# Performance work log

Measured on AMD Instinct MI355X. Metric: run time of the kernel, lower is better.

The kernel has to match this reference:

```python
import jax, jax.numpy as jnp
import numpy as np

BSZ, D = 256, 512
LOGIT_SCALE = 1.0


def setup_inputs() -> dict:
    key = jax.random.key(0)
    k1, k2, k3 = jax.random.split(key, 3)
    x = jax.random.normal(k1, (BSZ, D), dtype=jnp.float32)
    y = jax.random.normal(k2, (BSZ, D), dtype=jnp.float32)
    z = jax.random.normal(k3, (BSZ, D), dtype=jnp.float32)
    return {"x": x, "y": y, "z": z}


def _logits_n_squared(anchor, a, b, shift):
    # torch recursion: products[i*bsz + r] = a[r] * roll(b, i)[r] = a[r] * b[(r - i) % bsz]
    bsz = anchor.shape[0]
    P = a[None, :, :] * b[shift]              # (i, r, d) = (bsz, bsz, d)
    logits = jnp.einsum('ad,ird->air', anchor, P)  # (a, i, r)
    return LOGIT_SCALE * logits.reshape(bsz, bsz * bsz)


def _cross_entropy_diag(logits):
    bsz = logits.shape[0]
    lp = jax.nn.log_softmax(logits, axis=-1)
    idx = jnp.arange(bsz)
    return -jnp.mean(lp[idx, idx])


def reference(x, y, z):
    bsz = x.shape[0]
    r = jnp.arange(bsz)
    shift = (r[None, :] - r[:, None]) % bsz   # (i, r): index into b after roll by i
    reps = [x, y, z]
    losses = []
    for i in range(3):
        anchor = reps[i]
        non_anchor = [reps[j] for j in range(3) if j != i]
        logits = _logits_n_squared(anchor, non_anchor[0], non_anchor[1], shift)
        losses.append(_cross_entropy_diag(logits))
    return sum(losses) / 3.0
```

## Files before the change

### kernel.cpp

```cpp
#include <hip/hip_runtime.h>

#define DIM 512
#define BK 32
#define ASTRIDE 40

typedef unsigned int uint;
typedef unsigned short ushort;
typedef __attribute__((ext_vector_type(8))) short short8;
typedef __attribute__((ext_vector_type(4))) float f32x4;

__device__ __forceinline__ uint pack_bf16(float a, float b) {
    union { float f; uint u; } ua, ub;
    ua.f = a; ub.f = b;
    uint x0 = ua.u + 0x8000u;
    uint x1 = ub.u + 0x8000u;
    return __builtin_amdgcn_perm(x1, x0, 0x07060302);
}

__global__ void zconv_kernel(const float* __restrict__ z, ushort* __restrict__ zb) {
    int t = blockIdx.x * 256 + threadIdx.x;
    int f = t * 8;
    float4 a = *(const float4*)(z + f);
    float4 b = *(const float4*)(z + f + 4);
    uint4 o;
    o.x = pack_bf16(a.x, a.y);
    o.y = pack_bf16(a.z, a.w);
    o.z = pack_bf16(b.x, b.y);
    o.w = pack_bf16(b.z, b.w);
    *(uint4*)(zb + f) = o;
}

__global__ void __launch_bounds__(512, 4)
gemm_fused(const float* __restrict__ x, const float* __restrict__ y,
           const ushort* __restrict__ zb, const float* __restrict__ z,
           float* __restrict__ rowM, float* __restrict__ rowS,
           float* __restrict__ colM, float* __restrict__ colS,
           float* __restrict__ diag, uint* __restrict__ counter) {
    __shared__ __align__(16) float xs[DIM];
    __shared__ __align__(16) ushort As[128 * ASTRIDE];
    __shared__ __align__(16) ushort Bs[256 * BK];
    __shared__ float redA[128 * 4];
    __shared__ float rowMaxS[128];
    __shared__ float redB[256 * 2];
    __shared__ float colMaxS[256];
    __shared__ float dred[8];

    const int tid = threadIdx.x;
    const int a   = blockIdx.x >> 1;
    const int rt  = blockIdx.x & 1;

    if (blockIdx.x == 0 && tid == 0) *counter = 0u;

    xs[tid] = x[a * DIM + tid];

    const int lane = tid & 63;
    const int wave = tid >> 6;
    const int quad = lane >> 4;
    const int ln15 = lane & 15;
    const int wr = wave >> 2;
    const int wc = wave & 3;

    if (rt == 0) {
        float p = xs[tid] * y[a * DIM + tid] * z[a * DIM + tid];
        #pragma unroll
        for (int m = 1; m < 64; m <<= 1) p += __shfl_xor(p, m, 64);
        if (lane == 0) dred[wave] = p;
        __syncthreads();
        if (tid == 0) {
            float s = 0.f;
            #pragma unroll
            for (int w2 = 0; w2 < 8; ++w2) s += dred[w2];
            diag[a] = s;
        }
    }

    f32x4 acc[4][4];
    #pragma unroll
    for (int i = 0; i < 4; ++i)
        #pragma unroll
        for (int j = 0; j < 4; ++j)
            acc[i][j] = (f32x4){0.f, 0.f, 0.f, 0.f};

    const int rA = tid >> 2;
    const int kA = (tid & 3) * 8;
    const float* yrow = y + (rt * 128 + rA) * DIM + kA;

    const int s0 = wave * 128 + lane;
    const int row0 = s0 >> 2, kc0 = ((s0 & 3) - (row0 >> 1)) & 3;
    const ushort* gB0 = zb + row0 * DIM + kc0 * 8;
    const int s1 = s0 + 64;
    const int row1 = s1 >> 2, kc1 = ((s1 & 3) - (row1 >> 1)) & 3;
    const ushort* gB1 = zb + row1 * DIM + kc1 * 8;

    for (int kt = 0; kt < DIM / BK; ++kt) {
        const int k0 = kt * BK;
        __syncthreads();
        __builtin_amdgcn_global_load_lds(
            (const __attribute__((address_space(1))) void*)(gB0 + k0),
            (__attribute__((address_space(3))) void*)(Bs + wave * 1024), 16, 0, 0);
        __builtin_amdgcn_global_load_lds(
            (const __attribute__((address_space(1))) void*)(gB1 + k0),
            (__attribute__((address_space(3))) void*)(Bs + wave * 1024 + 512), 16, 0, 0);
        {
            float4 y0 = *(const float4*)(yrow + k0);
            float4 y1 = *(const float4*)(yrow + k0 + 4);
            float4 x0 = *(const float4*)(xs + k0 + kA);
            float4 x1 = *(const float4*)(xs + k0 + kA + 4);
            uint4 o;
            o.x = pack_bf16(y0.x * x0.x, y0.y * x0.y);
            o.y = pack_bf16(y0.z * x0.z, y0.w * x0.w);
            o.z = pack_bf16(y1.x * x1.x, y1.y * x1.y);
            o.w = pack_bf16(y1.z * x1.z, y1.w * x1.w);
            *(uint4*)(As + rA * ASTRIDE + kA) = o;
        }
        __syncthreads();
        short8 af[4], bfr[4];
        #pragma unroll
        for (int i = 0; i < 4; ++i)
            af[i] = *(const short8*)(As + (wr * 64 + i * 16 + ln15) * ASTRIDE + quad * 8);
        #pragma unroll
        for (int j = 0; j < 4; ++j) {
            int row = wc * 64 + j * 16 + ln15;
            int pos = row * 4 + ((quad + (row >> 1)) & 3);
            bfr[j] = *(const short8*)(Bs + pos * 8);
        }
        #pragma unroll
        for (int i = 0; i < 4; ++i)
            #pragma unroll
            for (int j = 0; j < 4; ++j)
                acc[i][j] = __builtin_amdgcn_mfma_f32_16x16x32_bf16(af[i], bfr[j], acc[i][j], 0, 0, 0);
    }
    __syncthreads();

    #pragma unroll
    for (int i = 0; i < 4; ++i) {
        #pragma unroll
        for (int reg = 0; reg < 4; ++reg) {
            float m = fmaxf(fmaxf(acc[i][0][reg], acc[i][1][reg]),
                            fmaxf(acc[i][2][reg], acc[i][3][reg]));
            #pragma unroll
            for (int d = 1; d < 16; d <<= 1) m = fmaxf(m, __shfl_xor(m, d, 64));
            if (ln15 == 0) redA[(wr * 64 + i * 16 + quad * 4 + reg) * 4 + wc] = m;
        }
    }
    __syncthreads();
    if (tid < 128) {
        float m = fmaxf(fmaxf(redA[tid * 4 + 0], redA[tid * 4 + 1]),
                        fmaxf(redA[tid * 4 + 2], redA[tid * 4 + 3]));
        rowMaxS[tid] = m;
    }
    __syncthreads();
    #pragma unroll
    for (int i = 0; i < 4; ++i) {
        #pragma unroll
        for (int reg = 0; reg < 4; ++reg) {
            int r = wr * 64 + i * 16 + quad * 4 + reg;
            float rm = rowMaxS[r];
            float s = __expf(acc[i][0][reg] - rm) + __expf(acc[i][1][reg] - rm)
                    + __expf(acc[i][2][reg] - rm) + __expf(acc[i][3][reg] - rm);
            #pragma unroll
            for (int d = 1; d < 16; d <<= 1) s += __shfl_xor(s, d, 64);
            if (ln15 == 0) redA[r * 4 + wc] = s;
        }
    }
    __syncthreads();
    if (tid < 128) {
        float s = redA[tid * 4 + 0] + redA[tid * 4 + 1] + redA[tid * 4 + 2] + redA[tid * 4 + 3];
        int rg = rt * 128 + tid;
        rowM[a * 256 + rg] = rowMaxS[tid];
        rowS[a * 256 + rg] = s;
    }

    #pragma unroll
    for (int j = 0; j < 4; ++j) {
        float m = -3.4e38f;
        #pragma unroll
        for (int i = 0; i < 4; ++i)
            #pragma unroll
            for (int reg = 0; reg < 4; ++reg)
                m = fmaxf(m, acc[i][j][reg]);
        m = fmaxf(m, __shfl_xor(m, 16, 64));
        m = fmaxf(m, __shfl_xor(m, 32, 64));
        if (quad == 0) redB[(wc * 64 + j * 16 + ln15) * 2 + wr] = m;
    }
    __syncthreads();
    if (tid < 256) colMaxS[tid] = fmaxf(redB[tid * 2], redB[tid * 2 + 1]);
    __syncthreads();
    #pragma unroll
    for (int j = 0; j < 4; ++j) {
        int n = wc * 64 + j * 16 + ln15;
        float cm = colMaxS[n];
        float s = 0.f;
        #pragma unroll
        for (int i = 0; i < 4; ++i)
            #pragma unroll
            for (int reg = 0; reg < 4; ++reg)
                s += __expf(acc[i][j][reg] - cm);
        s += __shfl_xor(s, 16, 64);
        s += __shfl_xor(s, 32, 64);
        if (quad == 0) redB[n * 2 + wr] = s;
    }
    __syncthreads();
    if (tid < 256) {
        float s = redB[tid * 2] + redB[tid * 2 + 1];
        colM[(a * 256 + tid) * 2 + rt] = colMaxS[tid];
        colS[(a * 256 + tid) * 2 + rt] = s;
    }
}

__device__ __forceinline__ float blk_max(float v, float* sm) {
    #pragma unroll
    for (int d = 1; d < 64; d <<= 1) v = fmaxf(v, __shfl_xor(v, d, 64));
    __syncthreads();
    if ((threadIdx.x & 63) == 0) sm[threadIdx.x >> 6] = v;
    __syncthreads();
    return fmaxf(fmaxf(sm[0], sm[1]), fmaxf(sm[2], sm[3]));
}
__device__ __forceinline__ float blk_sum(float v, float* sm) {
    #pragma unroll
    for (int d = 1; d < 64; d <<= 1) v += __shfl_xor(v, d, 64);
    __syncthreads();
    if ((threadIdx.x & 63) == 0) sm[threadIdx.x >> 6] = v;
    __syncthreads();
    return sm[0] + sm[1] + sm[2] + sm[3];
}

__global__ void combine_final(const float* __restrict__ rowM, const float* __restrict__ rowS,
                              const float* __restrict__ colM, const float* __restrict__ colS,
                              const float* __restrict__ diag,
                              float* __restrict__ m123, uint* __restrict__ counter,
                              float* __restrict__ out) {
    __shared__ float sm[4];
    __shared__ uint isLast;
    int b = blockIdx.x, t = threadIdx.x;
    float m = rowM[b * 256 + t], s = rowS[b * 256 + t];
    float M = blk_max(m, sm);
    float S = blk_sum(s * __expf(m - M), sm);
    float M1 = M + __logf(S);
    m = rowM[t * 256 + b]; s = rowS[t * 256 + b];
    M = blk_max(m, sm);
    S = blk_sum(s * __expf(m - M), sm);
    float M2 = M + __logf(S);
    float am = colM[(t * 256 + b) * 2 + 0], av = colS[(t * 256 + b) * 2 + 0];
    float bm = colM[(t * 256 + b) * 2 + 1], bv = colS[(t * 256 + b) * 2 + 1];
    m = fmaxf(am, bm);
    s = av * __expf(am - m) + bv * __expf(bm - m);
    M = blk_max(m, sm);
    S = blk_sum(s * __expf(m - M), sm);
    float M3 = M + __logf(S);
    if (t == 0) {
        m123[b] = M1 + M2 + M3;
        __threadfence();
        isLast = (atomicAdd(counter, 1u) == 255u) ? 1u : 0u;
    }
    __syncthreads();
    if (isLast) {
        __threadfence();
        const volatile float* vm = (const volatile float*)m123;
        const volatile float* vd = (const volatile float*)diag;
        float S1 = blk_sum(vm[t], sm);
        float S2 = blk_sum(vd[t], sm);
        if (t == 0) out[0] = S1 / 768.0f - S2 / 256.0f;
    }
}

extern "C" void kernel_launch(void* const* d_in, const int* in_sizes, int n_in,
                              void* d_out, int out_size, void* d_ws, size_t ws_size,
                              hipStream_t stream) {
    const float* x = (const float*)d_in[0];
    const float* y = (const float*)d_in[1];
    const float* z = (const float*)d_in[2];
    char* w = (char*)d_ws;
    ushort* zb  = (ushort*)(w);
    float* rowM = (float*)(w + 262144);
    float* rowS = (float*)(w + 524288);
    float* colM = (float*)(w + 786432);
    float* colS = (float*)(w + 1310720);
    float* diag = (float*)(w + 1835008);
    float* m123 = (float*)(w + 1836032);
    uint*  counter = (uint*)(w + 1837056);
    float* out  = (float*)d_out;

    zconv_kernel<<<64, 256, 0, stream>>>(z, zb);
    gemm_fused<<<512, 512, 0, stream>>>(x, y, zb, z, rowM, rowS, colM, colS, diag, counter);
    combine_final<<<256, 256, 0, stream>>>(rowM, rowS, colM, colS, diag, m123, counter, out);
}
```

Before: 101.0 us.

## Double-buffer A and B LDS tiles to overlap loads with MFMA

Doubles the shared-memory A and B tiles and prefetches the next K-slice (async global-to-LDS copies for z, register-prefetched y rows multiplied by x and packed to bf16) while the current slice runs through MFMA. This removes one barrier per iteration and hides global load latency behind compute. The cost is about twice the LDS for the tiles, which may lower occupancy against the 4-blocks-per-SM launch bound, plus extra registers for the prefetched y values.

```diff
diff --git a/kernel.cpp b/kernel.cpp
--- a/kernel.cpp
+++ b/kernel.cpp
@@ -8,6 +8,10 @@
 typedef unsigned short ushort;
 typedef __attribute__((ext_vector_type(8))) short short8;
 typedef __attribute__((ext_vector_type(4))) float f32x4;
+
+#define GLOAD_LDS(g, l) __builtin_amdgcn_global_load_lds( \
+    (const __attribute__((address_space(1))) void*)(g), \
+    (__attribute__((address_space(3))) void*)(l), 16, 0, 0)
 
 __device__ __forceinline__ uint pack_bf16(float a, float b) {
     union { float f; uint u; } ua, ub;
@@ -37,8 +41,8 @@
            float* __restrict__ colM, float* __restrict__ colS,
            float* __restrict__ diag, uint* __restrict__ counter) {
     __shared__ __align__(16) float xs[DIM];
-    __shared__ __align__(16) ushort As[128 * ASTRIDE];
-    __shared__ __align__(16) ushort Bs[256 * BK];
+    __shared__ __align__(16) ushort As[2][128 * ASTRIDE];
+    __shared__ __align__(16) ushort Bs[2][256 * BK];
     __shared__ float redA[128 * 4];
     __shared__ float rowMaxS[128];
     __shared__ float redB[256 * 2];
@@ -73,6 +77,7 @@
             diag[a] = s;
         }
     }
+    __syncthreads();
 
     f32x4 acc[4][4];
     #pragma unroll
@@ -92,43 +97,61 @@
     const int row1 = s1 >> 2, kc1 = ((s1 & 3) - (row1 >> 1)) & 3;
     const ushort* gB1 = zb + row1 * DIM + kc1 * 8;
 
-    for (int kt = 0; kt < DIM / BK; ++kt) {
-        const int k0 = kt * BK;
+    GLOAD_LDS(gB0, &Bs[0][wave * 1024]);
+    GLOAD_LDS(gB1, &Bs[0][wave * 1024 + 512]);
+    float4 ya = *(const float4*)(yrow);
+    float4 yb = *(const float4*)(yrow + 4);
+    {
+        float4 x0 = *(const float4*)(xs + kA);
+        float4 x1 = *(const float4*)(xs + kA + 4);
+        uint4 o;
+        o.x = pack_bf16(ya.x * x0.x, ya.y * x0.y);
+        o.y = pack_bf16(ya.z * x0.z, ya.w * x0.w);
+        o.z = pack_bf16(yb.x * x1.x, yb.y * x1.y);
+        o.w = pack_bf16(yb.z * x1.z, yb.w * x1.w);
+        *(uint4*)(&As[0][rA * ASTRIDE + kA]) = o;
+    }
+    ya = *(const float4*)(yrow + 32);
+    yb = *(const float4*)(yrow + 36);
+
+    #pragma unroll 2
+    for (int kt = 0; kt < 16; ++kt) {
+        const int cur = kt & 1, nxt = cur ^ 1;
         __syncthreads();
-        __builtin_amdgcn_global_load_lds(
-            (const __attribute__((address_space(1))) void*)(gB0 + k0),
-            (__attribute__((address_space(3))) void*)(Bs + wave * 1024), 16, 0, 0);
-        __builtin_amdgcn_global_load_lds(
-            (const __attribute__((address_space(1))) void*)(gB1 + k0),
-            (__attribute__((address_space(3))) void*)(Bs + wave * 1024 + 512), 16, 0, 0);
-        {
-            float4 y0 = *(const float4*)(yrow + k0);
-            float4 y1 = *(const float4*)(yrow + k0 + 4);
-            float4 x0 = *(const float4*)(xs + k0 + kA);
-            float4 x1 = *(const float4*)(xs + k0 + kA + 4);
-            uint4 o;
-            o.x = pack_bf16(y0.x * x0.x, y0.y * x0.y);
-            o.y = pack_bf16(y0.z * x0.z, y0.w * x0.w);
-            o.z = pack_bf16(y1.x * x1.x, y1.y * x1.y);
-            o.w = pack_bf16(y1.z * x1.z, y1.w * x1.w);
-            *(uint4*)(As + rA * ASTRIDE + kA) = o;
-        }
-        __syncthreads();
+        if (kt < 15) {
+            GLOAD_LDS(gB0 + (kt + 1) * 32, &Bs[nxt][wave * 1024]);
+            GLOAD_LDS(gB1 + (kt + 1) * 32, &Bs[nxt][wave * 1024 + 512]);
+        }
         short8 af[4], bfr[4];
         #pragma unroll
         for (int i = 0; i < 4; ++i)
-            af[i] = *(const short8*)(As + (wr * 64 + i * 16 + ln15) * ASTRIDE + quad * 8);
+            af[i] = *(const short8*)(&As[cur][(wr * 64 + i * 16 + ln15) * ASTRIDE + quad * 8]);
         #pragma unroll
         for (int j = 0; j < 4; ++j) {
             int row = wc * 64 + j * 16 + ln15;
             int pos = row * 4 + ((quad + (row >> 1)) & 3);
-            bfr[j] = *(const short8*)(Bs + pos * 8);
+            bfr[j] = *(const short8*)(&Bs[cur][pos * 8]);
         }
         #pragma unroll
         for (int i = 0; i < 4; ++i)
             #pragma unroll
             for (int j = 0; j < 4; ++j)
                 acc[i][j] = __builtin_amdgcn_mfma_f32_16x16x32_bf16(af[i], bfr[j], acc[i][j], 0, 0, 0);
+        if (kt < 15) {
+            const int k1 = (kt + 1) * 32;
+            float4 x0 = *(const float4*)(xs + k1 + kA);
+            float4 x1 = *(const float4*)(xs + k1 + kA + 4);
+            uint4 o;
+            o.x = pack_bf16(ya.x * x0.x, ya.y * x0.y);
+            o.y = pack_bf16(ya.z * x0.z, ya.w * x0.w);
+            o.z = pack_bf16(yb.x * x1.x, yb.y * x1.y);
+            o.w = pack_bf16(yb.z * x1.z, yb.w * x1.w);
+            *(uint4*)(&As[nxt][rA * ASTRIDE + kA]) = o;
+            if (kt < 14) {
+                ya = *(const float4*)(yrow + (kt + 2) * 32);
+                yb = *(const float4*)(yrow + (kt + 2) * 32 + 4);
+            }
+        }
     }
     __syncthreads();
 
```

New measurement: 99.22 us. Within noise of the previous version (-1.8%).

## Pre-swizzle y and z into MFMA fragment layout and drop LDS staging

Applied to the files above, without the earlier changes.

A prep kernel now converts both y and z to bf16 and stores them in a layout that matches the MFMA fragment order, so each lane can load its operand fragments straight from global memory. The GEMM loop no longer stages tiles in LDS and no longer needs per-iteration barriers. The x scaling is applied in registers by unpacking the bf16 y value, multiplying by x and repacking. This removes shared-memory traffic and synchronisation, but y is now rounded to bf16 twice, and every wave reads its fragments directly from global or L2 with no reuse through LDS.

```diff
diff --git a/kernel.cpp b/kernel.cpp
--- a/kernel.cpp
+++ b/kernel.cpp
@@ -1,8 +1,6 @@
 #include <hip/hip_runtime.h>
 
 #define DIM 512
-#define BK 32
-#define ASTRIDE 40
 
 typedef unsigned int uint;
 typedef unsigned short ushort;
@@ -17,28 +15,43 @@
     return __builtin_amdgcn_perm(x1, x0, 0x07060302);
 }
 
-__global__ void zconv_kernel(const float* __restrict__ z, ushort* __restrict__ zb) {
+__device__ __forceinline__ uint mul_pack(uint u, float xl, float xh) {
+    union { float f; uint u; } lo, hi, a, b;
+    lo.u = u << 16;
+    hi.u = u & 0xffff0000u;
+    a.f = lo.f * xl;
+    b.f = hi.f * xh;
+    return __builtin_amdgcn_perm(b.u + 0x8000u, a.u + 0x8000u, 0x07060302);
+}
+
+__global__ void conv_swizzle(const float* __restrict__ z, const float* __restrict__ y,
+                             ushort* __restrict__ zbf, ushort* __restrict__ ybf) {
     int t = blockIdx.x * 256 + threadIdx.x;
-    int f = t * 8;
-    float4 a = *(const float4*)(z + f);
-    float4 b = *(const float4*)(z + f + 4);
+    int idx = t & 16383;
+    const float* src = (t < 16384) ? z : y;
+    ushort* dst = (t < 16384) ? zbf : ybf;
+    int r15  = idx & 15;
+    int quad = (idx >> 4) & 3;
+    int kt   = (idx >> 6) & 15;
+    int g    = idx >> 10;
+    const float* p = src + (g * 16 + r15) * DIM + kt * 32 + quad * 8;
+    float4 a = *(const float4*)(p);
+    float4 b = *(const float4*)(p + 4);
     uint4 o;
     o.x = pack_bf16(a.x, a.y);
     o.y = pack_bf16(a.z, a.w);
     o.z = pack_bf16(b.x, b.y);
     o.w = pack_bf16(b.z, b.w);
-    *(uint4*)(zb + f) = o;
+    *(uint4*)(dst + idx * 8) = o;
 }
 
 __global__ void __launch_bounds__(512, 4)
 gemm_fused(const float* __restrict__ x, const float* __restrict__ y,
-           const ushort* __restrict__ zb, const float* __restrict__ z,
+           const float* __restrict__ z,
+           const ushort* __restrict__ ybf, const ushort* __restrict__ zbf,
            float* __restrict__ rowM, float* __restrict__ rowS,
            float* __restrict__ colM, float* __restrict__ colS,
            float* __restrict__ diag, uint* __restrict__ counter) {
-    __shared__ __align__(16) float xs[DIM];
-    __shared__ __align__(16) ushort As[128 * ASTRIDE];
-    __shared__ __align__(16) ushort Bs[256 * BK];
     __shared__ float redA[128 * 4];
     __shared__ float rowMaxS[128];
     __shared__ float redB[256 * 2];
@@ -50,8 +63,6 @@
     const int rt  = blockIdx.x & 1;
 
     if (blockIdx.x == 0 && tid == 0) *counter = 0u;
-
-    xs[tid] = x[a * DIM + tid];
 
     const int lane = tid & 63;
     const int wave = tid >> 6;
@@ -61,17 +72,17 @@
     const int wc = wave & 3;
 
     if (rt == 0) {
-        float p = xs[tid] * y[a * DIM + tid] * z[a * DIM + tid];
+        float p = x[a * DIM + tid] * y[a * DIM + tid] * z[a * DIM + tid];
         #pragma unroll
         for (int m = 1; m < 64; m <<= 1) p += __shfl_xor(p, m, 64);
         if (lane == 0) dred[wave] = p;
-        __syncthreads();
-        if (tid == 0) {
-            float s = 0.f;
-            #pragma unroll
-            for (int w2 = 0; w2 < 8; ++w2) s += dred[w2];
-            diag[a] = s;
-        }
+    }
+    __syncthreads();
+    if (rt == 0 && tid == 0) {
+        float s = 0.f;
+        #pragma unroll
+        for (int w2 = 0; w2 < 8; ++w2) s += dred[w2];
+        diag[a] = s;
     }
 
     f32x4 acc[4][4];
@@ -81,48 +92,34 @@
         for (int j = 0; j < 4; ++j)
             acc[i][j] = (f32x4){0.f, 0.f, 0.f, 0.f};
 
-    const int rA = tid >> 2;
-    const int kA = (tid & 3) * 8;
-    const float* yrow = y + (rt * 128 + rA) * DIM + kA;
-
-    const int s0 = wave * 128 + lane;
-    const int row0 = s0 >> 2, kc0 = ((s0 & 3) - (row0 >> 1)) & 3;
-    const ushort* gB0 = zb + row0 * DIM + kc0 * 8;
-    const int s1 = s0 + 64;
-    const int row1 = s1 >> 2, kc1 = ((s1 & 3) - (row1 >> 1)) & 3;
-    const ushort* gB1 = zb + row1 * DIM + kc1 * 8;
-
-    for (int kt = 0; kt < DIM / BK; ++kt) {
-        const int k0 = kt * BK;
-        __syncthreads();
-        __builtin_amdgcn_global_load_lds(
-            (const __attribute__((address_space(1))) void*)(gB0 + k0),
-            (__attribute__((address_space(3))) void*)(Bs + wave * 1024), 16, 0, 0);
-        __builtin_amdgcn_global_load_lds(
-            (const __attribute__((address_space(1))) void*)(gB1 + k0),
-            (__attribute__((address_space(3))) void*)(Bs + wave * 1024 + 512), 16, 0, 0);
-        {
-            float4 y0 = *(const float4*)(yrow + k0);
-            float4 y1 = *(const float4*)(yrow + k0 + 4);
-            float4 x0 = *(const float4*)(xs + k0 + kA);
-            float4 x1 = *(const float4*)(xs + k0 + kA + 4);
+    const ushort* ybase = ybf + (rt * 8 + wr * 4) * 8192 + lane * 8;
+    const ushort* zbase = zbf + (wc * 4) * 8192 + lane * 8;
+    const float*  xrow  = x + a * DIM + quad * 8;
+
+    #pragma unroll 2
+    for (int kt = 0; kt < 16; ++kt) {
+        uint4 zu[4], yu[4];
+        #pragma unroll
+        for (int j = 0; j < 4; ++j)
+            zu[j] = *(const uint4*)(zbase + j * 8192 + kt * 512);
+        #pragma unroll
+        for (int i = 0; i < 4; ++i)
+            yu[i] = *(const uint4*)(ybase + i * 8192 + kt * 512);
+        float4 x0 = *(const float4*)(xrow + kt * 32);
+        float4 x1 = *(const float4*)(xrow + kt * 32 + 4);
+
+        short8 af[4], bfr[4];
+        #pragma unroll
+        for (int j = 0; j < 4; ++j)
+            bfr[j] = *(short8*)&zu[j];
+        #pragma unroll
+        for (int i = 0; i < 4; ++i) {
             uint4 o;
-            o.x = pack_bf16(y0.x * x0.x, y0.y * x0.y);
-            o.y = pack_bf16(y0.z * x0.z, y0.w * x0.w);
-            o.z = pack_bf16(y1.x * x1.x, y1.y * x1.y);
-            o.w = pack_bf16(y1.z * x1.z, y1.w * x1.w);
-            *(uint4*)(As + rA * ASTRIDE + kA) = o;
-        }
-        __syncthreads();
-        short8 af[4], bfr[4];
-        #pragma unroll
-        for (int i = 0; i < 4; ++i)
-            af[i] = *(const short8*)(As + (wr * 64 + i * 16 + ln15) * ASTRIDE + quad * 8);
-        #pragma unroll
-        for (int j = 0; j < 4; ++j) {
-            int row = wc * 64 + j * 16 + ln15;
-            int pos = row * 4 + ((quad + (row >> 1)) & 3);
-            bfr[j] = *(const short8*)(Bs + pos * 8);
+            o.x = mul_pack(yu[i].x, x0.x, x0.y);
+            o.y = mul_pack(yu[i].y, x0.z, x0.w);
+            o.z = mul_pack(yu[i].z, x1.x, x1.y);
+            o.w = mul_pack(yu[i].w, x1.z, x1.w);
+            af[i] = *(short8*)&o;
         }
         #pragma unroll
         for (int i = 0; i < 4; ++i)
@@ -271,17 +268,18 @@
     const float* y = (const float*)d_in[1];
     const float* z = (const float*)d_in[2];
     char* w = (char*)d_ws;
-    ushort* zb  = (ushort*)(w);
-    float* rowM = (float*)(w + 262144);
-    float* rowS = (float*)(w + 524288);
-    float* colM = (float*)(w + 786432);
-    float* colS = (float*)(w + 1310720);
-    float* diag = (float*)(w + 1835008);
-    float* m123 = (float*)(w + 1836032);
-    uint*  counter = (uint*)(w + 1837056);
+    ushort* zbf = (ushort*)(w);
+    ushort* ybf = (ushort*)(w + 262144);
+    float* rowM = (float*)(w + 524288);
+    float* rowS = (float*)(w + 786432);
+    float* colM = (float*)(w + 1048576);
+    float* colS = (float*)(w + 1572864);
+    float* diag = (float*)(w + 2097152);
+    float* m123 = (float*)(w + 2098176);
+    uint*  counter = (uint*)(w + 2099200);
     float* out  = (float*)d_out;
 
-    zconv_kernel<<<64, 256, 0, stream>>>(z, zb);
-    gemm_fused<<<512, 512, 0, stream>>>(x, y, zb, z, rowM, rowS, colM, colS, diag, counter);
+    conv_swizzle<<<128, 256, 0, stream>>>(z, y, zbf, ybf);
+    gemm_fused<<<512, 512, 0, stream>>>(x, y, z, ybf, zbf, rowM, rowS, colM, colS, diag, counter);
     combine_final<<<256, 256, 0, stream>>>(rowM, rowS, colM, colS, diag, m123, counter, out);
 }
```

Measured after the change: 111.7 us. 10.6% more time.
